# Kernel optimization log

Measured on AMD Instinct MI355X. Metric: run time of the kernel, lower is better.

Reference implementation:

```python
import jax, jax.numpy as jnp
import numpy as np

B, S, E, H = 2, 2048, 1024, 16
DH = E // H


def setup_inputs() -> dict:
    key = jax.random.key(0)
    ks = jax.random.split(key, 7)
    sc = 1.0 / np.sqrt(E)
    return {
        "x": jax.random.normal(ks[0], (B, S, E), dtype=jnp.float32),
        "Wq": jax.random.uniform(ks[1], (E, E), jnp.float32, -sc, sc),
        "bq": jax.random.uniform(ks[2], (E,), jnp.float32, -sc, sc),
        "Wk": jax.random.uniform(ks[3], (E, E), jnp.float32, -sc, sc),
        "bk": jax.random.uniform(ks[4], (E,), jnp.float32, -sc, sc),
        "Wv": jax.random.uniform(ks[5], (E, E), jnp.float32, -sc, sc),
        "bv": jax.random.uniform(ks[6], (E,), jnp.float32, -sc, sc),
    }


def reference(x, Wq, bq, Wk, bk, Wv, bv):
    b, s, _ = x.shape
    # torch Linear: y = x @ W.T + b
    q = (x @ Wq.T + bq).reshape(b, s, H, DH).transpose(0, 2, 1, 3)  # [B,H,S,Dh]
    k = (x @ Wk.T + bk).reshape(b, s, H, DH).transpose(0, 2, 1, 3)
    v = (x @ Wv.T + bv).reshape(b, s, H, DH).transpose(0, 2, 1, 3)
    # original einsum labels treat axis1 as 's' and axis2 as 'h'/'v':
    # scores: [B, S_q, H, S_k]  (softmax over keys, last axis)
    scores = jnp.einsum('bshd,bsvd->bhsv', q, k) / np.sqrt(DH)
    probs = jax.nn.softmax(scores, axis=-1)
    # out: [B, H, S, Dh] per original label permutation
    out = jnp.einsum('bhsv,bsvd->bshd', probs, v)
    # original reshapes WITHOUT transposing heads back (faithful quirk)
    return out.reshape(b, s, E)
```

## Files before the change

### kernel.cpp

```cpp
#include <hip/hip_runtime.h>
#include <hip/hip_bf16.h>

#define Bb 2
#define Ss 2048
#define Ee 1024
#define Hh 16
#define Dh 64
#define QSCALE 0.18033688011112042f

using u16 = unsigned short;
using u32 = unsigned int;
typedef __attribute__((ext_vector_type(8))) short short8;
typedef __attribute__((ext_vector_type(8))) u16 ushort8;
typedef __attribute__((ext_vector_type(4))) float f32x4;
typedef __attribute__((ext_vector_type(16))) float f32x16;
typedef __attribute__((ext_vector_type(4))) u32 uint4v;

#define GAS __attribute__((address_space(1)))
#define LAS __attribute__((address_space(3)))

__device__ __forceinline__ void gload16(const u16* g, u16* l) {
  __builtin_amdgcn_global_load_lds((const GAS unsigned int*)g,
                                   (LAS unsigned int*)l, 16, 0, 0);
}

__device__ __forceinline__ u16 f2bf(float f) {
  union { float f; unsigned u; } v;
  v.f = f;
  unsigned u = v.u;
  unsigned r = (u + 0x7FFFu + ((u >> 16) & 1u)) >> 16;
  return (u16)r;
}

__global__ __launch_bounds__(256) void cvt_all(
    const float* __restrict__ x, const float* __restrict__ wq,
    const float* __restrict__ wk, const float* __restrict__ wv,
    u16* __restrict__ xo, u16* __restrict__ wqo, u16* __restrict__ wko,
    u16* __restrict__ wvo) {
  const int b = blockIdx.x;
  const float* s;
  u16* d;
  int i;
  if (b < 2048) {
    s = x; d = xo; i = b * 256 + threadIdx.x;
  } else {
    const int wb = b - 2048;
    const int which = wb >> 9;
    s = which == 0 ? wq : (which == 1 ? wk : wv);
    d = which == 0 ? wqo : (which == 1 ? wko : wvo);
    i = (wb & 511) * 256 + threadIdx.x;
  }
  const float* p = s + (size_t)i * 8;
  ushort8 o;
#pragma unroll
  for (int j = 0; j < 8; ++j) o[j] = f2bf(p[j]);
  *(ushort8*)(d + (size_t)i * 8) = o;
}

__global__ __launch_bounds__(256) void qkv_gemm(
    const u16* __restrict__ Xb, const u16* __restrict__ Wcat,
    const float* __restrict__ bq, const float* __restrict__ bk,
    const float* __restrict__ bv,
    u16* __restrict__ Qo, u16* __restrict__ Ko, u16* __restrict__ Vo) {
  __shared__ u16 Ast[2][128][32];
  __shared__ u16 Bst[2][128][32];
  const int tid = threadIdx.x;
  const int lane = tid & 63;
  const int w = tid >> 6;
  const int wm = w >> 1, wn = w & 1;
  const int c = lane & 15, g = lane >> 4;
  const int flat = blockIdx.x;
  const int xcd = flat & 7;
  const int loc = flat >> 3;
  const int m_blk = (xcd >> 1) * 8 + (loc & 7);
  const int n_blk = (xcd & 1) * 12 + (loc >> 3);
  const int m0 = m_blk * 128;
  const int n0 = n_blk * 128;
  const bool swapv = n0 >= 2048;

  f32x4 acc[4][4] = {};

#pragma unroll
  for (int i = 0; i < 2; ++i) {
    const int elem = i * 2048 + tid * 8;
    const int row = elem >> 5, col = elem & 31;
    const int lbase = i * 2048 + w * 512;
    gload16(Xb + (size_t)(m0 + row) * 1024 + col, &Ast[0][0][0] + lbase);
    gload16(Wcat + (size_t)(n0 + row) * 1024 + col, &Bst[0][0][0] + lbase);
  }

  for (int kt = 0; kt < 32; ++kt) {
    __syncthreads();
    if (kt < 31) {
      const int k0n = (kt + 1) * 32;
      const int nb = (kt + 1) & 1;
#pragma unroll
      for (int i = 0; i < 2; ++i) {
        const int elem = i * 2048 + tid * 8;
        const int row = elem >> 5, col = elem & 31;
        const int lbase = i * 2048 + w * 512;
        gload16(Xb + (size_t)(m0 + row) * 1024 + k0n + col,
                &Ast[nb][0][0] + lbase);
        gload16(Wcat + (size_t)(n0 + row) * 1024 + k0n + col,
                &Bst[nb][0][0] + lbase);
      }
    }
    const int cb = kt & 1;

    short8 af[4], bf[4];
#pragma unroll
    for (int mf = 0; mf < 4; ++mf)
      af[mf] = *(const short8*)&Ast[cb][wm * 64 + mf * 16 + c][g * 8];
#pragma unroll
    for (int nf = 0; nf < 4; ++nf)
      bf[nf] = *(const short8*)&Bst[cb][wn * 64 + nf * 16 + c][g * 8];
    if (!swapv) {
#pragma unroll
      for (int mf = 0; mf < 4; ++mf)
#pragma unroll
        for (int nf = 0; nf < 4; ++nf)
          acc[mf][nf] = __builtin_amdgcn_mfma_f32_16x16x32_bf16(
              af[mf], bf[nf], acc[mf][nf], 0, 0, 0);
    } else {
#pragma unroll
      for (int mf = 0; mf < 4; ++mf)
#pragma unroll
        for (int nf = 0; nf < 4; ++nf)
          acc[mf][nf] = __builtin_amdgcn_mfma_f32_16x16x32_bf16(
              bf[nf], af[mf], acc[mf][nf], 0, 0, 0);
    }
  }

  if (!swapv) {
    const int which = n0 >> 10;
    u16* Oo = which == 0 ? Qo : Ko;
    const float* bias = which == 0 ? bq : bk;
    const float scl = which == 0 ? QSCALE : 1.0f;
#pragma unroll
    for (int nf = 0; nf < 4; ++nf) {
      const int n = (n0 & 1023) + wn * 64 + nf * 16 + c;
      const float bval = bias[n];
      const int hh = n >> 6, dd = n & 63;
#pragma unroll
      for (int mf = 0; mf < 4; ++mf) {
#pragma unroll
        for (int r = 0; r < 4; ++r) {
          const int m = m0 + wm * 64 + mf * 16 + g * 4 + r;
          const int bb = m >> 11, ss = m & 2047;
          Oo[(((size_t)bb * Hh + hh) * Ss + ss) * Dh + dd] =
              f2bf((acc[mf][nf][r] + bval) * scl);
        }
      }
    }
  } else {
#pragma unroll
    for (int nf = 0; nf < 4; ++nf) {
#pragma unroll
      for (int r = 0; r < 4; ++r) {
        const int n = (n0 - 2048) + wn * 64 + nf * 16 + g * 4 + r;
        const float bval = bv[n];
        const int hh = n >> 6, dd = n & 63;
#pragma unroll
        for (int mf = 0; mf < 4; ++mf) {
          const int m = m0 + wm * 64 + mf * 16 + c;
          const int bb = m >> 11, ss = m & 2047;
          Vo[(((size_t)bb * Hh + hh) * Dh + dd) * Ss + ss] =
              f2bf(acc[mf][nf][r] + bval);
        }
      }
    }
  }
}

__global__ __launch_bounds__(256, 2) void attn(
    const u16* __restrict__ Q, const u16* __restrict__ K,
    const u16* __restrict__ VT, float* __restrict__ out) {
  __shared__ u16 Kst[2][2][64][64];
  __shared__ u16 Vst[2][2][64][64];
  const int tid = threadIdx.x;
  const int lane = tid & 63;
  const int w = tid >> 6;
  const int c5 = lane & 31, g2 = lane >> 5;
  const int flat = blockIdx.x;
  const int bh = (flat & 7) * 4 + ((flat >> 3) >> 4);
  const int q0 = ((flat >> 3) & 15) * 128;
  const u16* Qb = Q + (size_t)bh * Ss * Dh;
  const u16* Kb = K + (size_t)bh * Ss * Dh;
  const u16* VTb = VT + (size_t)bh * Ss * Dh;

  const int srow = lane >> 3;
  const int scolx = ((lane & 7) * 8) ^ (srow * 8);

  const u16* Qrow = Qb + (size_t)(q0 + w * 32 + c5) * Dh + 8 * g2;
  short8 qf[4];
#pragma unroll
  for (int s = 0; s < 4; ++s) qf[s] = *(const short8*)(Qrow + 16 * s);

  short8 ones;
#pragma unroll
  for (int j = 0; j < 8; ++j) ones[j] = (short)0x3F80;
  f32x16 ZZ = {};

  const int cxor = (c5 & 7) << 4;
  int slot[4];
#pragma unroll
  for (int s = 0; s < 4; ++s) slot[s] = c5 * 128 + ((32 * s + 16 * g2) ^ cxor);

#pragma unroll
  for (int sub = 0; sub < 2; ++sub) {
#pragma unroll
    for (int p = 0; p < 2; ++p) {
      const int row = w * 8 + srow + p * 32;
      gload16(Kb + (size_t)(sub * 64 + row) * Dh + scolx,
              &Kst[0][sub][0][0] + w * 512 + p * 2048);
      gload16(VTb + (size_t)row * Ss + sub * 64 + scolx,
              &Vst[0][sub][0][0] + w * 512 + p * 2048);
    }
  }

  f32x16 oacc0 = {}, oacc1 = {}, lacc = {};

  for (int kt = 0; kt < 16; ++kt) {
    __syncthreads();
    if (kt < 15) {
      const int k0n = (kt + 1) * 128;
      const int nb = (kt + 1) & 1;
#pragma unroll
      for (int sub = 0; sub < 2; ++sub) {
#pragma unroll
        for (int p = 0; p < 2; ++p) {
          const int row = w * 8 + srow + p * 32;
          gload16(Kb + (size_t)(k0n + sub * 64 + row) * Dh + scolx,
                  &Kst[nb][sub][0][0] + w * 512 + p * 2048);
          gload16(VTb + (size_t)row * Ss + k0n + sub * 64 + scolx,
                  &Vst[nb][sub][0][0] + w * 512 + p * 2048);
        }
      }
    }
    const char* kb0 = (const char*)&Kst[kt & 1][0][0][0];
    const char* kb1 = (const char*)&Kst[kt & 1][1][0][0];
    const char* vb0 = (const char*)&Vst[kt & 1][0][0][0];
    const char* vb1 = (const char*)&Vst[kt & 1][1][0][0];

    f32x16 sA0, sA1, sB0, sB1;
    __builtin_amdgcn_s_setprio(1);
    {
      short8 ka0 = *(const short8*)(kb0 + slot[0]);
      short8 ka1 = *(const short8*)(kb0 + slot[0] + 4096);
      short8 kc0 = *(const short8*)(kb1 + slot[0]);
      short8 kc1 = *(const short8*)(kb1 + slot[0] + 4096);
      sA0 = __builtin_amdgcn_mfma_f32_32x32x16_bf16(ka0, qf[0], ZZ, 0, 0, 0);
      sA1 = __builtin_amdgcn_mfma_f32_32x32x16_bf16(ka1, qf[0], ZZ, 0, 0, 0);
      sB0 = __builtin_amdgcn_mfma_f32_32x32x16_bf16(kc0, qf[0], ZZ, 0, 0, 0);
      sB1 = __builtin_amdgcn_mfma_f32_32x32x16_bf16(kc1, qf[0], ZZ, 0, 0, 0);
    }
#pragma unroll
    for (int s = 1; s < 4; ++s) {
      short8 ka0 = *(const short8*)(kb0 + slot[s]);
      short8 ka1 = *(const short8*)(kb0 + slot[s] + 4096);
      short8 kc0 = *(const short8*)(kb1 + slot[s]);
      short8 kc1 = *(const short8*)(kb1 + slot[s] + 4096);
      sA0 = __builtin_amdgcn_mfma_f32_32x32x16_bf16(ka0, qf[s], sA0, 0, 0, 0);
      sA1 = __builtin_amdgcn_mfma_f32_32x32x16_bf16(ka1, qf[s], sA1, 0, 0, 0);
      sB0 = __builtin_amdgcn_mfma_f32_32x32x16_bf16(kc0, qf[s], sB0, 0, 0, 0);
      sB1 = __builtin_amdgcn_mfma_f32_32x32x16_bf16(kc1, qf[s], sB1, 0, 0, 0);
    }
    __builtin_amdgcn_s_setprio(0);

    u32 pkvA[2][8];
#pragma unroll
    for (int i = 0; i < 8; ++i) {
      const u32 e0 = __builtin_bit_cast(u32, __builtin_amdgcn_exp2f(sA0[2 * i]));
      const u32 e1 = __builtin_bit_cast(u32, __builtin_amdgcn_exp2f(sA0[2 * i + 1]));
      pkvA[0][i] = __builtin_amdgcn_perm(e1, e0, 0x07060302u);
    }
#pragma unroll
    for (int i = 0; i < 8; ++i) {
      const u32 e0 = __builtin_bit_cast(u32, __builtin_amdgcn_exp2f(sA1[2 * i]));
      const u32 e1 = __builtin_bit_cast(u32, __builtin_amdgcn_exp2f(sA1[2 * i + 1]));
      pkvA[1][i] = __builtin_amdgcn_perm(e1, e0, 0x07060302u);
    }

    __builtin_amdgcn_s_setprio(1);
#pragma unroll
    for (int sp = 0; sp < 4; ++sp) {
      const int kb = sp >> 1, sg = sp & 1;
      u32 x0 = pkvA[kb][4 * sg + 0], y0 = pkvA[kb][4 * sg + 2];
      u32 x1 = pkvA[kb][4 * sg + 1], y1 = pkvA[kb][4 * sg + 3];
      asm("v_permlane32_swap_b32 %0, %1" : "+v"(x0), "+v"(y0));
      asm("v_permlane32_swap_b32 %0, %1" : "+v"(x1), "+v"(y1));
      uint4v av;
      av[0] = x0; av[1] = x1; av[2] = y0; av[3] = y1;
      const short8 af = __builtin_bit_cast(short8, av);
      short8 vf0 = *(const short8*)(vb0 + slot[sp]);
      short8 vf1 = *(const short8*)(vb0 + slot[sp] + 4096);
      lacc = __builtin_amdgcn_mfma_f32_32x32x16_bf16(af, ones, lacc, 0, 0, 0);
      oacc0 = __builtin_amdgcn_mfma_f32_32x32x16_bf16(af, vf0, oacc0, 0, 0, 0);
      oacc1 = __builtin_amdgcn_mfma_f32_32x32x16_bf16(af, vf1, oacc1, 0, 0, 0);
    }
    __builtin_amdgcn_s_setprio(0);

    u32 pkvB[2][8];
#pragma unroll
    for (int i = 0; i < 8; ++i) {
      const u32 e0 = __builtin_bit_cast(u32, __builtin_amdgcn_exp2f(sB0[2 * i]));
      const u32 e1 = __builtin_bit_cast(u32, __builtin_amdgcn_exp2f(sB0[2 * i + 1]));
      pkvB[0][i] = __builtin_amdgcn_perm(e1, e0, 0x07060302u);
    }
#pragma unroll
    for (int i = 0; i < 8; ++i) {
      const u32 e0 = __builtin_bit_cast(u32, __builtin_amdgcn_exp2f(sB1[2 * i]));
      const u32 e1 = __builtin_bit_cast(u32, __builtin_amdgcn_exp2f(sB1[2 * i + 1]));
      pkvB[1][i] = __builtin_amdgcn_perm(e1, e0, 0x07060302u);
    }

    __builtin_amdgcn_s_setprio(1);
#pragma unroll
    for (int sp = 0; sp < 4; ++sp) {
      const int kb = sp >> 1, sg = sp & 1;
      u32 x0 = pkvB[kb][4 * sg + 0], y0 = pkvB[kb][4 * sg + 2];
      u32 x1 = pkvB[kb][4 * sg + 1], y1 = pkvB[kb][4 * sg + 3];
      asm("v_permlane32_swap_b32 %0, %1" : "+v"(x0), "+v"(y0));
      asm("v_permlane32_swap_b32 %0, %1" : "+v"(x1), "+v"(y1));
      uint4v av;
      av[0] = x0; av[1] = x1; av[2] = y0; av[3] = y1;
      const short8 af = __builtin_bit_cast(short8, av);
      short8 vf0 = *(const short8*)(vb1 + slot[sp]);
      short8 vf1 = *(const short8*)(vb1 + slot[sp] + 4096);
      lacc = __builtin_amdgcn_mfma_f32_32x32x16_bf16(af, ones, lacc, 0, 0, 0);
      oacc0 = __builtin_amdgcn_mfma_f32_32x32x16_bf16(af, vf0, oacc0, 0, 0, 0);
      oacc1 = __builtin_amdgcn_mfma_f32_32x32x16_bf16(af, vf1, oacc1, 0, 0, 0);
    }
    __builtin_amdgcn_s_setprio(0);
  }

  float* ob = out + (size_t)bh * Ss * Dh;
#pragma unroll
  for (int r = 0; r < 16; ++r) {
    const float inv = 1.0f / lacc[r];
    const int q = q0 + w * 32 + (r & 3) + 8 * (r >> 2) + 4 * g2;
    ob[(size_t)q * Dh + c5] = oacc0[r] * inv;
    ob[(size_t)q * Dh + 32 + c5] = oacc1[r] * inv;
  }
}

extern "C" void kernel_launch(void* const* d_in, const int* in_sizes, int n_in,
                              void* d_out, int out_size, void* d_ws, size_t ws_size,
                              hipStream_t stream) {
  const float* x = (const float*)d_in[0];
  const float* Wq = (const float*)d_in[1];
  const float* bq = (const float*)d_in[2];
  const float* Wk = (const float*)d_in[3];
  const float* bk = (const float*)d_in[4];
  const float* Wv = (const float*)d_in[5];
  const float* bv = (const float*)d_in[6];
  float* out = (float*)d_out;

  if (ws_size < (size_t)(38u << 20)) return;
  char* ws = (char*)d_ws;
  u16* Qb = (u16*)(ws + (size_t)(0u << 20));
  u16* Kb = (u16*)(ws + (size_t)(8u << 20));
  u16* Vb = (u16*)(ws + (size_t)(16u << 20));
  u16* Xb = (u16*)(ws + (size_t)(24u << 20));
  u16* Wqb = (u16*)(ws + (size_t)(32u << 20));
  u16* Wkb = (u16*)(ws + (size_t)(34u << 20));
  u16* Wvb = (u16*)(ws + (size_t)(36u << 20));

  cvt_all<<<3584, 256, 0, stream>>>(x, Wq, Wk, Wv, Xb, Wqb, Wkb, Wvb);
  qkv_gemm<<<768, 256, 0, stream>>>(Xb, Wqb, bq, bk, bv, Qb, Kb, Vb);
  attn<<<512, 256, 0, stream>>>(Qb, Kb, Vb, out);
}
```

Before: 108.0 us.

## Enlarge QKV GEMM tile to 128x384 with 8 waves per block

The QKV projection GEMM now uses 128x384 output tiles computed by 512-thread blocks (2x4 waves, each holding a 64x96 accumulator). The grid shrinks from 768 to 256 blocks, which is exactly one wave of blocks on the GPU, and the old XCD-aware block swizzle is dropped. Each loaded X tile is reused across three times as many output columns, which is meant to cut global and LDS traffic. In exchange, register pressure per wave rises and a block can span both the K and V regions, so the Q/K-versus-V branch is now taken per 16-column fragment. The barrier also moves from the start to the end of each k-iteration.

```diff
diff --git a/kernel.cpp b/kernel.cpp
--- a/kernel.cpp
+++ b/kernel.cpp
@@ -57,90 +57,91 @@
   *(ushort8*)(d + (size_t)i * 8) = o;
 }
 
-__global__ __launch_bounds__(256) void qkv_gemm(
+__global__ __launch_bounds__(512, 2) void qkv_gemm(
     const u16* __restrict__ Xb, const u16* __restrict__ Wcat,
     const float* __restrict__ bq, const float* __restrict__ bk,
     const float* __restrict__ bv,
     u16* __restrict__ Qo, u16* __restrict__ Ko, u16* __restrict__ Vo) {
   __shared__ u16 Ast[2][128][32];
-  __shared__ u16 Bst[2][128][32];
+  __shared__ u16 Bst[2][384][32];
   const int tid = threadIdx.x;
   const int lane = tid & 63;
   const int w = tid >> 6;
-  const int wm = w >> 1, wn = w & 1;
+  const int wm = w >> 2, wn = w & 3;
   const int c = lane & 15, g = lane >> 4;
   const int flat = blockIdx.x;
-  const int xcd = flat & 7;
-  const int loc = flat >> 3;
-  const int m_blk = (xcd >> 1) * 8 + (loc & 7);
-  const int n_blk = (xcd & 1) * 12 + (loc >> 3);
-  const int m0 = m_blk * 128;
-  const int n0 = n_blk * 128;
-  const bool swapv = n0 >= 2048;
-
-  f32x4 acc[4][4] = {};
-
-#pragma unroll
-  for (int i = 0; i < 2; ++i) {
-    const int elem = i * 2048 + tid * 8;
-    const int row = elem >> 5, col = elem & 31;
-    const int lbase = i * 2048 + w * 512;
-    gload16(Xb + (size_t)(m0 + row) * 1024 + col, &Ast[0][0][0] + lbase);
-    gload16(Wcat + (size_t)(n0 + row) * 1024 + col, &Bst[0][0][0] + lbase);
-  }
+  const int m0 = (flat >> 3) * 128;
+  const int n0 = (flat & 7) * 384;
+
+  bool isv[6];
+#pragma unroll
+  for (int nf = 0; nf < 6; ++nf) isv[nf] = (n0 + wn * 96 + nf * 16) >= 2048;
+
+  f32x4 acc[4][6] = {};
+
+  {
+    const int elemA = tid * 8;
+    gload16(Xb + (size_t)(m0 + (elemA >> 5)) * 1024 + (elemA & 31),
+            &Ast[0][0][0] + w * 512);
+#pragma unroll
+    for (int i = 0; i < 3; ++i) {
+      const int elem = i * 4096 + tid * 8;
+      gload16(Wcat + (size_t)(n0 + (elem >> 5)) * 1024 + (elem & 31),
+              &Bst[0][0][0] + i * 4096 + w * 512);
+    }
+  }
+  __syncthreads();
 
   for (int kt = 0; kt < 32; ++kt) {
-    __syncthreads();
     if (kt < 31) {
       const int k0n = (kt + 1) * 32;
       const int nb = (kt + 1) & 1;
-#pragma unroll
-      for (int i = 0; i < 2; ++i) {
-        const int elem = i * 2048 + tid * 8;
-        const int row = elem >> 5, col = elem & 31;
-        const int lbase = i * 2048 + w * 512;
-        gload16(Xb + (size_t)(m0 + row) * 1024 + k0n + col,
-                &Ast[nb][0][0] + lbase);
-        gload16(Wcat + (size_t)(n0 + row) * 1024 + k0n + col,
-                &Bst[nb][0][0] + lbase);
+      const int elemA = tid * 8;
+      gload16(Xb + (size_t)(m0 + (elemA >> 5)) * 1024 + k0n + (elemA & 31),
+              &Ast[nb][0][0] + w * 512);
+#pragma unroll
+      for (int i = 0; i < 3; ++i) {
+        const int elem = i * 4096 + tid * 8;
+        gload16(Wcat + (size_t)(n0 + (elem >> 5)) * 1024 + k0n + (elem & 31),
+                &Bst[nb][0][0] + i * 4096 + w * 512);
       }
     }
     const int cb = kt & 1;
-
-    short8 af[4], bf[4];
+    short8 af[4], bf[6];
 #pragma unroll
     for (int mf = 0; mf < 4; ++mf)
       af[mf] = *(const short8*)&Ast[cb][wm * 64 + mf * 16 + c][g * 8];
 #pragma unroll
-    for (int nf = 0; nf < 4; ++nf)
-      bf[nf] = *(const short8*)&Bst[cb][wn * 64 + nf * 16 + c][g * 8];
-    if (!swapv) {
-#pragma unroll
-      for (int mf = 0; mf < 4; ++mf)
-#pragma unroll
-        for (int nf = 0; nf < 4; ++nf)
+    for (int nf = 0; nf < 6; ++nf)
+      bf[nf] = *(const short8*)&Bst[cb][wn * 96 + nf * 16 + c][g * 8];
+#pragma unroll
+    for (int nf = 0; nf < 6; ++nf) {
+      if (isv[nf]) {
+#pragma unroll
+        for (int mf = 0; mf < 4; ++mf)
+          acc[mf][nf] = __builtin_amdgcn_mfma_f32_16x16x32_bf16(
+              bf[nf], af[mf], acc[mf][nf], 0, 0, 0);
+      } else {
+#pragma unroll
+        for (int mf = 0; mf < 4; ++mf)
           acc[mf][nf] = __builtin_amdgcn_mfma_f32_16x16x32_bf16(
               af[mf], bf[nf], acc[mf][nf], 0, 0, 0);
-    } else {
-#pragma unroll
-      for (int mf = 0; mf < 4; ++mf)
-#pragma unroll
-        for (int nf = 0; nf < 4; ++nf)
-          acc[mf][nf] = __builtin_amdgcn_mfma_f32_16x16x32_bf16(
-              bf[nf], af[mf], acc[mf][nf], 0, 0, 0);
-    }
-  }
-
-  if (!swapv) {
-    const int which = n0 >> 10;
-    u16* Oo = which == 0 ? Qo : Ko;
-    const float* bias = which == 0 ? bq : bk;
-    const float scl = which == 0 ? QSCALE : 1.0f;
-#pragma unroll
-    for (int nf = 0; nf < 4; ++nf) {
-      const int n = (n0 & 1023) + wn * 64 + nf * 16 + c;
-      const float bval = bias[n];
-      const int hh = n >> 6, dd = n & 63;
+      }
+    }
+    __syncthreads();
+  }
+
+#pragma unroll
+  for (int nf = 0; nf < 6; ++nf) {
+    const int nc0 = n0 + wn * 96 + nf * 16;
+    if (nc0 < 2048) {
+      const int which = nc0 >> 10;
+      u16* Oo = which == 0 ? Qo : Ko;
+      const float* bias = which == 0 ? bq : bk;
+      const float scl = which == 0 ? QSCALE : 1.0f;
+      const int ncol = (nc0 & 1023) + c;
+      const float bval = bias[ncol];
+      const int hh = ncol >> 6, dd = ncol & 63;
 #pragma unroll
       for (int mf = 0; mf < 4; ++mf) {
 #pragma unroll
@@ -151,15 +152,12 @@
               f2bf((acc[mf][nf][r] + bval) * scl);
         }
       }
-    }
-  } else {
-#pragma unroll
-    for (int nf = 0; nf < 4; ++nf) {
+    } else {
 #pragma unroll
       for (int r = 0; r < 4; ++r) {
-        const int n = (n0 - 2048) + wn * 64 + nf * 16 + g * 4 + r;
-        const float bval = bv[n];
-        const int hh = n >> 6, dd = n & 63;
+        const int ncol = (nc0 - 2048) + g * 4 + r;
+        const float bval = bv[ncol];
+        const int hh = ncol >> 6, dd = ncol & 63;
 #pragma unroll
         for (int mf = 0; mf < 4; ++mf) {
           const int m = m0 + wm * 64 + mf * 16 + c;
@@ -367,6 +365,6 @@
   u16* Wvb = (u16*)(ws + (size_t)(36u << 20));
 
   cvt_all<<<3584, 256, 0, stream>>>(x, Wq, Wk, Wv, Xb, Wqb, Wkb, Wvb);
-  qkv_gemm<<<768, 256, 0, stream>>>(Xb, Wqb, bq, bk, bv, Qb, Kb, Vb);
+  qkv_gemm<<<256, 512, 0, stream>>>(Xb, Wqb, bq, bk, bv, Qb, Kb, Vb);
   attn<<<512, 256, 0, stream>>>(Qb, Kb, Vb, out);
 }
```

Result: faster. 99.38 us, median of 3 (-8.0%).
